# Kernel tuning notes

Hardware: AMD Instinct MI355X
Metric: run time of the kernel (lower is better)

## Reference

```python
import jax, jax.numpy as jnp
import numpy as np

LAMBDA = 10.0      # sinkhorn_lambda from init_kwargs
N_ITERS = 100      # fixed Sinkhorn iteration count
B, T_MAX, D_MAX = 256, 256, 256
TP, DP = T_MAX + 1, D_MAX + 1   # expanded with births/deaths row+col
L = TP * DP                      # padded flat output length per example
EPS = 1e-12


def setup_inputs() -> dict:
    key = jax.random.key(0)
    k1, k2, k3 = jax.random.split(key, 3)
    affinity_scores = jax.random.uniform(k1, (B, T_MAX, D_MAX), dtype=jnp.float32)
    num_detections = jax.random.randint(k2, (B,), 32, D_MAX + 1, dtype=jnp.int32)
    num_tracklets = jax.random.randint(k3, (B,), 32, T_MAX + 1, dtype=jnp.int32)
    return {
        "affinity_scores": affinity_scores,
        "num_detections": num_detections,
        "num_tracklets": num_tracklets,
    }


def _sinkhorn_transport(aff, nd, nt):
    """Masked Sinkhorn on the expanded (nt+1)x(nd+1) matrix, padded to [TP,DP]."""
    r = jnp.arange(TP)
    c = jnp.arange(DP)
    row_valid = r <= nt          # nt tracklet rows + 1 births/deaths row
    col_valid = c <= nd
    interior = (r[:, None] < nt) & (c[None, :] < nd)
    aff_pad = jnp.pad(aff, ((0, 1), (0, 1)))
    aff_e = jnp.where(interior, aff_pad, 0.0)   # dummy row/col have affinity 0
    mask = (row_valid[:, None] & col_valid[None, :]).astype(aff.dtype)
    # cost = -affinity  =>  kernel K = exp(-lambda * cost) = exp(lambda * affinity)
    K = jnp.exp(LAMBDA * aff_e) * mask
    ndf = nd.astype(aff.dtype)
    ntf = nt.astype(aff.dtype)
    # target marginals: [1,...,1, length] on valid entries, 0 on padding
    row_sums = jnp.where(r < nt, 1.0, jnp.where(r == nt, ndf, 0.0))
    col_sums = jnp.where(c < nd, 1.0, jnp.where(c == nd, ntf, 0.0))
    u0 = jnp.zeros((TP,), aff.dtype)
    v0 = col_valid.astype(aff.dtype)

    def body(carry, _):
        u, v = carry
        u = jnp.where(row_valid, row_sums / (K @ v + EPS), 0.0)
        v = jnp.where(col_valid, col_sums / (K.T @ u + EPS), 0.0)
        return (u, v), None

    (u, v), _ = jax.lax.scan(body, (u0, v0), None, length=N_ITERS)
    transport = u[:, None] * K * v[None, :]
    return transport, interior, row_valid, col_valid


def _single(aff, nd, nt):
    transport, interior, row_valid, col_valid = _sinkhorn_transport(aff, nd, nt)
    r = jnp.arange(TP)
    c = jnp.arange(DP)

    # hard assignment on transport[:-1,:-1] (valid interior): mutual argmax
    neg_inf = jnp.array(-jnp.inf, transport.dtype)
    t_in = jnp.where(interior, transport, neg_inf)
    row_max = jnp.max(t_in, axis=1, keepdims=True)
    col_max = jnp.max(t_in, axis=0, keepdims=True)
    assign_in = interior & (t_in == row_max) & (t_in == col_max)
    # births/deaths: unmatched tracklets -> death col nd; unmatched detections -> birth row nt
    row_has = jnp.any(assign_in, axis=1)
    col_has = jnp.any(assign_in, axis=0)
    deaths = (r[:, None] < nt) & (c[None, :] == nd) & (~row_has)[:, None]
    births = (r[:, None] == nt) & (c[None, :] < nd) & (~col_has)[None, :]
    assignment = assign_in | deaths | births

    # flatten the (nt+1)x(nd+1) valid submatrix row-major, zero-pad to length L
    k = jnp.arange(L)
    length = (nt + 1) * (nd + 1)
    rr = jnp.clip(k // (nd + 1), 0, T_MAX)
    cc = k % (nd + 1)
    valid = k < length
    t_flat = jnp.where(valid, transport[rr, cc], 0.0)
    a_flat = jnp.where(valid, assignment[rr, cc], False)
    return t_flat, a_flat


def reference(affinity_scores, num_detections, num_tracklets):
    t_flat, a_flat = jax.vmap(_single)(affinity_scores, num_detections, num_tracklets)
    return t_flat, a_flat
```

## Files before the change

### kernel.cpp

```cpp
#include <hip/hip_runtime.h>


#define T_MAX   256
#define L_FLAT  (257 * 257)
#define N_ITERS 100
#define LAMBDA_F 10.0f
#define EPS_F    1e-12f

#define QX1  0xB1
#define QX2  0x4E
#define ROR4 0x124
#define ROR8 0x128

template<int CTRL>
__device__ __forceinline__ float dpp_addf(float x) {
    int t = __builtin_amdgcn_update_dpp(0, __float_as_int(x), CTRL, 0xF, 0xF, true);
    return x + __int_as_float(t);
}
template<int CTRL>
__device__ __forceinline__ float dpp_maxf(float x) {
    int t = __builtin_amdgcn_update_dpp(0, __float_as_int(x), CTRL, 0xF, 0xF, true);
    return fmaxf(x, __int_as_float(t));
}
template<int CTRL>
__device__ __forceinline__ int dpp_ori(int x) {
    int t = __builtin_amdgcn_update_dpp(0, x, CTRL, 0xF, 0xF, true);
    return x | t;
}
__device__ __forceinline__ float swz16_addf(float x) {
    return x + __int_as_float(__builtin_amdgcn_ds_swizzle(__float_as_int(x), 0x401F));
}
__device__ __forceinline__ float swz16_maxf(float x) {
    return fmaxf(x, __int_as_float(__builtin_amdgcn_ds_swizzle(__float_as_int(x), 0x401F)));
}
__device__ __forceinline__ int swz16_ori(int x) {
    return x | __builtin_amdgcn_ds_swizzle(x, 0x401F);
}
__device__ __forceinline__ float sel4(float a, float b, float c, float d, int rg) {
    float lo = (rg & 1) ? b : a;
    float hi = (rg & 1) ? d : c;
    return (rg & 2) ? hi : lo;
}

__global__ __launch_bounds__(1024) void assoc_sinkhorn_kernel(
    const float* __restrict__ aff,
    const int*   __restrict__ ndet,
    const int*   __restrict__ ntrk,
    float*       __restrict__ out_t,
    float*       __restrict__ out_a)
{
    const int b   = blockIdx.x;
    const int nd  = ndet[b];
    const int nt  = ntrk[b];
    const int tid = threadIdx.x;
    const int w   = tid >> 6;
    const int l   = tid & 63;
    const int rg  = l & 3;
    const int cg  = l >> 2;
    const int R0  = (w << 4) + (rg << 2);
    const int C0  = cg << 4;

    __shared__ __align__(16) float red[16 * 256];
    __shared__ __align__(16) float varr[256];
    __shared__ __align__(16) float cmax_s[256];
    __shared__ __align__(16) float supart[16];
    __shared__ __align__(16) float svpart[2][4];
    __shared__ float sc_vbd;
    __shared__ float sc_ubd;

    float K[4][16];
    {
        const float* Ab = aff + (size_t)b * (T_MAX * T_MAX);
        #pragma unroll
        for (int i = 0; i < 4; ++i) {
            const int r = R0 + i;
            const float* row = Ab + (size_t)r * T_MAX + C0;
            #pragma unroll
            for (int k = 0; k < 4; ++k) {
                const float4 x = *reinterpret_cast<const float4*>(row + 4 * k);
                const float a4[4] = {x.x, x.y, x.z, x.w};
                #pragma unroll
                for (int e = 0; e < 4; ++e) {
                    const int j = 4 * k + e;
                    const bool interior = (r < nt) && ((C0 + j) < nd);
                    K[i][j] = interior ? expf(LAMBDA_F * a4[e]) : 0.0f;
                }
            }
        }
    }

    if (tid < 256) varr[tid] = (tid < nd) ? 1.0f : 0.0f;
    if (tid == 0) {
        sc_vbd = 1.0f;
        svpart[0][0] = (float)nd; svpart[0][1] = 0.f; svpart[0][2] = 0.f; svpart[0][3] = 0.f;
    }
    __syncthreads();

    float u[4] = {0.f, 0.f, 0.f, 0.f};
    float vbd_reg = 1.0f;

    for (int it = 0; it < N_ITERS; ++it) {
        const float vbd = sc_vbd;
        float v[16];
        {
            const float4 a0 = *reinterpret_cast<const float4*>(&varr[C0]);
            const float4 a1 = *reinterpret_cast<const float4*>(&varr[C0 + 4]);
            const float4 a2 = *reinterpret_cast<const float4*>(&varr[C0 + 8]);
            const float4 a3 = *reinterpret_cast<const float4*>(&varr[C0 + 12]);
            v[0]=a0.x; v[1]=a0.y; v[2]=a0.z; v[3]=a0.w;
            v[4]=a1.x; v[5]=a1.y; v[6]=a1.z; v[7]=a1.w;
            v[8]=a2.x; v[9]=a2.y; v[10]=a2.z; v[11]=a2.w;
            v[12]=a3.x; v[13]=a3.y; v[14]=a3.z; v[15]=a3.w;
        }
        float p[4];
        #pragma unroll
        for (int i = 0; i < 4; ++i) {
            float s = 0.f;
            #pragma unroll
            for (int j = 0; j < 16; ++j) s = fmaf(K[i][j], v[j], s);
            p[i] = s;
        }
        #pragma unroll
        for (int i = 0; i < 4; ++i) p[i] = dpp_addf<ROR4>(p[i]);
        #pragma unroll
        for (int i = 0; i < 4; ++i) p[i] = dpp_addf<ROR8>(p[i]);
        #pragma unroll
        for (int i = 0; i < 4; ++i) p[i] = swz16_addf(p[i]);
        #pragma unroll
        for (int i = 0; i < 4; ++i) p[i] += __shfl_xor(p[i], 32, 64);
        #pragma unroll
        for (int i = 0; i < 4; ++i)
            u[i] = ((R0 + i) < nt) ? 1.0f / (p[i] + vbd + EPS_F) : 0.0f;

        {
            float su = (u[0] + u[1]) + (u[2] + u[3]);
            su = dpp_addf<QX1>(su);
            su = dpp_addf<QX2>(su);
            if (l == 0) supart[w] = su;
        }

        float q[16];
        #pragma unroll
        for (int j = 0; j < 16; ++j) {
            float s = fmaf(K[0][j], u[0], 0.f);
            s = fmaf(K[1][j], u[1], s);
            s = fmaf(K[2][j], u[2], s);
            q[j] = fmaf(K[3][j], u[3], s);
        }
        #pragma unroll
        for (int j = 0; j < 16; ++j) q[j] = dpp_addf<QX1>(q[j]);
        #pragma unroll
        for (int j = 0; j < 16; ++j) q[j] = dpp_addf<QX2>(q[j]);
        {
            float4 o;
            o.x = sel4(q[0], q[4], q[8],  q[12], rg);
            o.y = sel4(q[1], q[5], q[9],  q[13], rg);
            o.z = sel4(q[2], q[6], q[10], q[14], rg);
            o.w = sel4(q[3], q[7], q[11], q[15], rg);
            *reinterpret_cast<float4*>(&red[w * 256 + C0 + (rg << 2)]) = o;
        }
        __syncthreads();

        if (tid < 256) {
            const int p_rd = it & 1;
            const float4 sv4 = *reinterpret_cast<const float4*>(&svpart[p_rd][0]);
            const float Sv = (sv4.x + sv4.y) + (sv4.z + sv4.w);
            const float ubd = (float)nd / (Sv + vbd_reg + EPS_F);

            float s0 = 0.f, s1 = 0.f, s2 = 0.f, s3 = 0.f;
            #pragma unroll
            for (int k = 0; k < 16; k += 4) {
                s0 += red[k * 256 + tid];
                s1 += red[(k + 1) * 256 + tid];
                s2 += red[(k + 2) * 256 + tid];
                s3 += red[(k + 3) * 256 + tid];
            }
            const float s = (s0 + s1) + (s2 + s3);

            const float4 p0 = *reinterpret_cast<const float4*>(&supart[0]);
            const float4 p1 = *reinterpret_cast<const float4*>(&supart[4]);
            const float4 p2 = *reinterpret_cast<const float4*>(&supart[8]);
            const float4 p3 = *reinterpret_cast<const float4*>(&supart[12]);
            const float Su = ((p0.x+p0.y)+(p0.z+p0.w)) + ((p1.x+p1.y)+(p1.z+p1.w))
                           + ((p2.x+p2.y)+(p2.z+p2.w)) + ((p3.x+p3.y)+(p3.z+p3.w));

            const float vn = (tid < nd) ? 1.0f / (s + ubd + EPS_F) : 0.0f;
            varr[tid] = vn;

            const float vbd_new = (float)nt / (Su + ubd + EPS_F);
            vbd_reg = vbd_new;
            if (tid == 0) { sc_vbd = vbd_new; sc_ubd = ubd; }

            float sv = vn;
            sv = dpp_addf<QX1>(sv);
            sv = dpp_addf<QX2>(sv);
            sv = dpp_addf<ROR4>(sv);
            sv = dpp_addf<ROR8>(sv);
            sv = swz16_addf(sv);
            sv += __shfl_xor(sv, 32, 64);
            if (l == 0) svpart[p_rd ^ 1][w] = sv;
        }
        __syncthreads();
    }

    const float vbdF = sc_vbd;
    const float ubdF = sc_ubd;
    float v[16];
    {
        const float4 a0 = *reinterpret_cast<const float4*>(&varr[C0]);
        const float4 a1 = *reinterpret_cast<const float4*>(&varr[C0 + 4]);
        const float4 a2 = *reinterpret_cast<const float4*>(&varr[C0 + 8]);
        const float4 a3 = *reinterpret_cast<const float4*>(&varr[C0 + 12]);
        v[0]=a0.x; v[1]=a0.y; v[2]=a0.z; v[3]=a0.w;
        v[4]=a1.x; v[5]=a1.y; v[6]=a1.z; v[7]=a1.w;
        v[8]=a2.x; v[9]=a2.y; v[10]=a2.z; v[11]=a2.w;
        v[12]=a3.x; v[13]=a3.y; v[14]=a3.z; v[15]=a3.w;
    }
    #pragma unroll
    for (int i = 0; i < 4; ++i) {
        #pragma unroll
        for (int j = 0; j < 16; ++j) K[i][j] = u[i] * K[i][j] * v[j];
    }

    float m[4];
    #pragma unroll
    for (int i = 0; i < 4; ++i) {
        float mm = K[i][0];
        #pragma unroll
        for (int j = 1; j < 16; ++j) mm = fmaxf(mm, K[i][j]);
        m[i] = mm;
    }
    #pragma unroll
    for (int i = 0; i < 4; ++i) m[i] = dpp_maxf<ROR4>(m[i]);
    #pragma unroll
    for (int i = 0; i < 4; ++i) m[i] = dpp_maxf<ROR8>(m[i]);
    #pragma unroll
    for (int i = 0; i < 4; ++i) m[i] = swz16_maxf(m[i]);
    #pragma unroll
    for (int i = 0; i < 4; ++i) m[i] = fmaxf(m[i], __shfl_xor(m[i], 32, 64));

    {
        float cmx[16];
        #pragma unroll
        for (int j = 0; j < 16; ++j)
            cmx[j] = fmaxf(fmaxf(K[0][j], K[1][j]), fmaxf(K[2][j], K[3][j]));
        #pragma unroll
        for (int j = 0; j < 16; ++j) cmx[j] = dpp_maxf<QX1>(cmx[j]);
        #pragma unroll
        for (int j = 0; j < 16; ++j) cmx[j] = dpp_maxf<QX2>(cmx[j]);
        float4 o;
        o.x = sel4(cmx[0], cmx[4], cmx[8],  cmx[12], rg);
        o.y = sel4(cmx[1], cmx[5], cmx[9],  cmx[13], rg);
        o.z = sel4(cmx[2], cmx[6], cmx[10], cmx[14], rg);
        o.w = sel4(cmx[3], cmx[7], cmx[11], cmx[15], rg);
        *reinterpret_cast<float4*>(&red[w * 256 + C0 + (rg << 2)]) = o;
    }
    __syncthreads();
    if (tid < 256) {
        float mm = red[tid];
        #pragma unroll
        for (int k = 1; k < 16; ++k) mm = fmaxf(mm, red[k * 256 + tid]);
        cmax_s[tid] = mm;
    }
    __syncthreads();

    float cm[16];
    {
        const float4 a0 = *reinterpret_cast<const float4*>(&cmax_s[C0]);
        const float4 a1 = *reinterpret_cast<const float4*>(&cmax_s[C0 + 4]);
        const float4 a2 = *reinterpret_cast<const float4*>(&cmax_s[C0 + 8]);
        const float4 a3 = *reinterpret_cast<const float4*>(&cmax_s[C0 + 12]);
        cm[0]=a0.x; cm[1]=a0.y; cm[2]=a0.z; cm[3]=a0.w;
        cm[4]=a1.x; cm[5]=a1.y; cm[6]=a1.z; cm[7]=a1.w;
        cm[8]=a2.x; cm[9]=a2.y; cm[10]=a2.z; cm[11]=a2.w;
        cm[12]=a3.x; cm[13]=a3.y; cm[14]=a3.z; cm[15]=a3.w;
    }
    unsigned bits[4];
    #pragma unroll
    for (int i = 0; i < 4; ++i) {
        unsigned bi = 0;
        const int r = R0 + i;
        #pragma unroll
        for (int j = 0; j < 16; ++j) {
            const int c = C0 + j;
            if ((r < nt) && (c < nd) && (K[i][j] == m[i]) && (K[i][j] == cm[j]))
                bi |= (1u << j);
        }
        bits[i] = bi;
    }
    int rh[4];
    #pragma unroll
    for (int i = 0; i < 4; ++i) rh[i] = bits[i] ? 1 : 0;
    #pragma unroll
    for (int i = 0; i < 4; ++i) rh[i] = dpp_ori<ROR4>(rh[i]);
    #pragma unroll
    for (int i = 0; i < 4; ++i) rh[i] = dpp_ori<ROR8>(rh[i]);
    #pragma unroll
    for (int i = 0; i < 4; ++i) rh[i] = swz16_ori(rh[i]);
    #pragma unroll
    for (int i = 0; i < 4; ++i) rh[i] |= __shfl_xor(rh[i], 32, 64);

    {
        const unsigned anyb = bits[0] | bits[1] | bits[2] | bits[3];
        float ch[16];
        #pragma unroll
        for (int j = 0; j < 16; ++j) ch[j] = ((anyb >> j) & 1u) ? 1.0f : 0.0f;
        #pragma unroll
        for (int j = 0; j < 16; ++j) ch[j] = dpp_maxf<QX1>(ch[j]);
        #pragma unroll
        for (int j = 0; j < 16; ++j) ch[j] = dpp_maxf<QX2>(ch[j]);
        float4 o;
        o.x = sel4(ch[0], ch[4], ch[8],  ch[12], rg);
        o.y = sel4(ch[1], ch[5], ch[9],  ch[13], rg);
        o.z = sel4(ch[2], ch[6], ch[10], ch[14], rg);
        o.w = sel4(ch[3], ch[7], ch[11], ch[15], rg);
        *reinterpret_cast<float4*>(&red[w * 256 + C0 + (rg << 2)]) = o;
    }
    __syncthreads();

    float* Ot = out_t + (size_t)b * L_FLAT;
    float* Oa = out_a + (size_t)b * L_FLAT;
    const int stride = nd + 1;

    if (tid < 256) {
        float c = red[tid];
        #pragma unroll
        for (int k = 1; k < 16; ++k) c = fmaxf(c, red[k * 256 + tid]);
        if (tid < nd) {
            const int kk = nt * stride + tid;
            Ot[kk] = ubdF * varr[tid];
            Oa[kk] = (c > 0.0f) ? 0.0f : 1.0f;
        }
    }
    if (tid == 0) {
        const int kk = nt * stride + nd;
        Ot[kk] = ubdF * vbdF;
        Oa[kk] = 0.0f;
    }
    if (cg == 0) {
        #pragma unroll
        for (int i = 0; i < 4; ++i) {
            const int r = R0 + i;
            if (r < nt) {
                const int kk = r * stride + nd;
                Ot[kk] = u[i] * vbdF;
                Oa[kk] = rh[i] ? 0.0f : 1.0f;
            }
        }
    }
    #pragma unroll
    for (int i = 0; i < 4; ++i) {
        const int r = R0 + i;
        if (r < nt) {
            const int base = r * stride;
            #pragma unroll
            for (int j = 0; j < 16; ++j) {
                const int c = C0 + j;
                if (c < nd) {
                    Ot[base + c] = K[i][j];
                    Oa[base + c] = ((bits[i] >> j) & 1u) ? 1.0f : 0.0f;
                }
            }
        }
    }
    const int length = (nt + 1) * stride;
    for (int k = length + tid; k < L_FLAT; k += 1024) {
        Ot[k] = 0.0f;
        Oa[k] = 0.0f;
    }
}

extern "C" void kernel_launch(void* const* d_in, const int* in_sizes, int n_in,
                              void* d_out, int out_size, void* d_ws, size_t ws_size,
                              hipStream_t stream)
{
    const float* aff  = (const float*)d_in[0];
    const int*   ndet = (const int*)d_in[1];
    const int*   ntrk = (const int*)d_in[2];
    const int    Bn   = in_sizes[1];
    float* out_t = (float*)d_out;
    float* out_a = out_t + (size_t)Bn * L_FLAT;
    assoc_sinkhorn_kernel<<<dim3(Bn), dim3(1024), 0, stream>>>(aff, ndet, ntrk, out_t, out_a);
}
```

Before: 444.6 us.

## Use packed FMA, fast reciprocal, and all-thread column reduction in Sinkhorn loop

```diff
diff --git a/kernel.cpp b/kernel.cpp
--- a/kernel.cpp
+++ b/kernel.cpp
@@ -1,11 +1,14 @@
 #include <hip/hip_runtime.h>
 
+
+typedef float v2f __attribute__((ext_vector_type(2)));
 
 #define T_MAX   256
 #define L_FLAT  (257 * 257)
 #define N_ITERS 100
 #define LAMBDA_F 10.0f
 #define EPS_F    1e-12f
+#define RS      260
 
 #define QX1  0xB1
 #define QX2  0x4E
@@ -36,10 +39,12 @@
 __device__ __forceinline__ int swz16_ori(int x) {
     return x | __builtin_amdgcn_ds_swizzle(x, 0x401F);
 }
-__device__ __forceinline__ float sel4(float a, float b, float c, float d, int rg) {
-    float lo = (rg & 1) ? b : a;
-    float hi = (rg & 1) ? d : c;
-    return (rg & 2) ? hi : lo;
+__device__ __forceinline__ float fast_rcp(float x) {
+#if __has_builtin(__builtin_amdgcn_rcpf)
+    return __builtin_amdgcn_rcpf(x);
+#else
+    return 1.0f / x;
+#endif
 }
 
 __global__ __launch_bounds__(1024) void assoc_sinkhorn_kernel(
@@ -60,15 +65,16 @@
     const int R0  = (w << 4) + (rg << 2);
     const int C0  = cg << 4;
 
-    __shared__ __align__(16) float red[16 * 256];
+    __shared__ __align__(16) float red[16 * RS];
     __shared__ __align__(16) float varr[256];
     __shared__ __align__(16) float cmax_s[256];
     __shared__ __align__(16) float supart[16];
-    __shared__ __align__(16) float svpart[2][4];
-    __shared__ float sc_vbd;
-    __shared__ float sc_ubd;
-
-    float K[4][16];
+    __shared__ __align__(16) float svpart[2][16];
+
+    const float ndf = (float)nd;
+    const float ntf = (float)nt;
+
+    v2f K2[4][8];
     {
         const float* Ab = aff + (size_t)b * (T_MAX * T_MAX);
         #pragma unroll
@@ -78,47 +84,48 @@
             #pragma unroll
             for (int k = 0; k < 4; ++k) {
                 const float4 x = *reinterpret_cast<const float4*>(row + 4 * k);
-                const float a4[4] = {x.x, x.y, x.z, x.w};
-                #pragma unroll
-                for (int e = 0; e < 4; ++e) {
-                    const int j = 4 * k + e;
-                    const bool interior = (r < nt) && ((C0 + j) < nd);
-                    K[i][j] = interior ? expf(LAMBDA_F * a4[e]) : 0.0f;
-                }
+                const bool rv = (r < nt);
+                const float e0 = (rv && (C0 + 4*k + 0) < nd) ? expf(LAMBDA_F * x.x) : 0.0f;
+                const float e1 = (rv && (C0 + 4*k + 1) < nd) ? expf(LAMBDA_F * x.y) : 0.0f;
+                const float e2 = (rv && (C0 + 4*k + 2) < nd) ? expf(LAMBDA_F * x.z) : 0.0f;
+                const float e3 = (rv && (C0 + 4*k + 3) < nd) ? expf(LAMBDA_F * x.w) : 0.0f;
+                K2[i][2*k + 0] = (v2f){e0, e1};
+                K2[i][2*k + 1] = (v2f){e2, e3};
             }
         }
     }
 
     if (tid < 256) varr[tid] = (tid < nd) ? 1.0f : 0.0f;
-    if (tid == 0) {
-        sc_vbd = 1.0f;
-        svpart[0][0] = (float)nd; svpart[0][1] = 0.f; svpart[0][2] = 0.f; svpart[0][3] = 0.f;
-    }
+    if (tid < 16)  svpart[0][tid] = (tid == 0) ? ndf : 0.0f;
     __syncthreads();
 
     float u[4] = {0.f, 0.f, 0.f, 0.f};
-    float vbd_reg = 1.0f;
+    float vbd = 1.0f;
+    float ubd = 0.0f;
+
+    const int s2c   = (w << 4) + (l >> 2);
+    const int s2sub = l & 3;
 
     for (int it = 0; it < N_ITERS; ++it) {
-        const float vbd = sc_vbd;
-        float v[16];
+        v2f v2[8];
         {
             const float4 a0 = *reinterpret_cast<const float4*>(&varr[C0]);
             const float4 a1 = *reinterpret_cast<const float4*>(&varr[C0 + 4]);
             const float4 a2 = *reinterpret_cast<const float4*>(&varr[C0 + 8]);
             const float4 a3 = *reinterpret_cast<const float4*>(&varr[C0 + 12]);
-            v[0]=a0.x; v[1]=a0.y; v[2]=a0.z; v[3]=a0.w;
-            v[4]=a1.x; v[5]=a1.y; v[6]=a1.z; v[7]=a1.w;
-            v[8]=a2.x; v[9]=a2.y; v[10]=a2.z; v[11]=a2.w;
-            v[12]=a3.x; v[13]=a3.y; v[14]=a3.z; v[15]=a3.w;
+            v2[0] = (v2f){a0.x, a0.y}; v2[1] = (v2f){a0.z, a0.w};
+            v2[2] = (v2f){a1.x, a1.y}; v2[3] = (v2f){a1.z, a1.w};
+            v2[4] = (v2f){a2.x, a2.y}; v2[5] = (v2f){a2.z, a2.w};
+            v2[6] = (v2f){a3.x, a3.y}; v2[7] = (v2f){a3.z, a3.w};
         }
         float p[4];
         #pragma unroll
         for (int i = 0; i < 4; ++i) {
-            float s = 0.f;
+            v2f s2 = K2[i][0] * v2[0];
             #pragma unroll
-            for (int j = 0; j < 16; ++j) s = fmaf(K[i][j], v[j], s);
-            p[i] = s;
+            for (int jj = 1; jj < 8; ++jj)
+                s2 = __builtin_elementwise_fma(K2[i][jj], v2[jj], s2);
+            p[i] = s2.x + s2.y;
         }
         #pragma unroll
         for (int i = 0; i < 4; ++i) p[i] = dpp_addf<ROR4>(p[i]);
@@ -128,9 +135,10 @@
         for (int i = 0; i < 4; ++i) p[i] = swz16_addf(p[i]);
         #pragma unroll
         for (int i = 0; i < 4; ++i) p[i] += __shfl_xor(p[i], 32, 64);
+        const float vbdE = vbd + EPS_F;
         #pragma unroll
         for (int i = 0; i < 4; ++i)
-            u[i] = ((R0 + i) < nt) ? 1.0f / (p[i] + vbd + EPS_F) : 0.0f;
+            u[i] = ((R0 + i) < nt) ? fast_rcp(p[i] + vbdE) : 0.0f;
 
         {
             float su = (u[0] + u[1]) + (u[2] + u[3]);
@@ -139,96 +147,99 @@
             if (l == 0) supart[w] = su;
         }
 
+        v2f q2[8];
+        {
+            const v2f u0 = (v2f){u[0], u[0]};
+            #pragma unroll
+            for (int jj = 0; jj < 8; ++jj) q2[jj] = K2[0][jj] * u0;
+            #pragma unroll
+            for (int i = 1; i < 4; ++i) {
+                const v2f ui = (v2f){u[i], u[i]};
+                #pragma unroll
+                for (int jj = 0; jj < 8; ++jj)
+                    q2[jj] = __builtin_elementwise_fma(K2[i][jj], ui, q2[jj]);
+            }
+        }
         float q[16];
         #pragma unroll
-        for (int j = 0; j < 16; ++j) {
-            float s = fmaf(K[0][j], u[0], 0.f);
-            s = fmaf(K[1][j], u[1], s);
-            s = fmaf(K[2][j], u[2], s);
-            q[j] = fmaf(K[3][j], u[3], s);
-        }
+        for (int jj = 0; jj < 8; ++jj) { q[2*jj] = q2[jj].x; q[2*jj + 1] = q2[jj].y; }
         #pragma unroll
         for (int j = 0; j < 16; ++j) q[j] = dpp_addf<QX1>(q[j]);
         #pragma unroll
         for (int j = 0; j < 16; ++j) q[j] = dpp_addf<QX2>(q[j]);
+        if (rg == 0) {
+            float* dst = &red[w * RS + C0];
+            *reinterpret_cast<float4*>(dst)      = make_float4(q[0],  q[1],  q[2],  q[3]);
+            *reinterpret_cast<float4*>(dst + 4)  = make_float4(q[4],  q[5],  q[6],  q[7]);
+            *reinterpret_cast<float4*>(dst + 8)  = make_float4(q[8],  q[9],  q[10], q[11]);
+            *reinterpret_cast<float4*>(dst + 12) = make_float4(q[12], q[13], q[14], q[15]);
+        }
+        __syncthreads();
+
         {
-            float4 o;
-            o.x = sel4(q[0], q[4], q[8],  q[12], rg);
-            o.y = sel4(q[1], q[5], q[9],  q[13], rg);
-            o.z = sel4(q[2], q[6], q[10], q[14], rg);
-            o.w = sel4(q[3], q[7], q[11], q[15], rg);
-            *reinterpret_cast<float4*>(&red[w * 256 + C0 + (rg << 2)]) = o;
+            const int p_rd = it & 1;
+            float s0 = red[(4*s2sub + 0) * RS + s2c];
+            float s1 = red[(4*s2sub + 1) * RS + s2c];
+            float s2 = red[(4*s2sub + 2) * RS + s2c];
+            float s3 = red[(4*s2sub + 3) * RS + s2c];
+            float s = (s0 + s1) + (s2 + s3);
+            s = dpp_addf<QX1>(s);
+            s = dpp_addf<QX2>(s);
+
+            const float4 a0 = *reinterpret_cast<const float4*>(&supart[0]);
+            const float4 a1 = *reinterpret_cast<const float4*>(&supart[4]);
+            const float4 a2 = *reinterpret_cast<const float4*>(&supart[8]);
+            const float4 a3 = *reinterpret_cast<const float4*>(&supart[12]);
+            const float Su = (((a0.x+a0.y)+(a0.z+a0.w)) + ((a1.x+a1.y)+(a1.z+a1.w)))
+                           + (((a2.x+a2.y)+(a2.z+a2.w)) + ((a3.x+a3.y)+(a3.z+a3.w)));
+            const float4 b0 = *reinterpret_cast<const float4*>(&svpart[p_rd][0]);
+            const float4 b1 = *reinterpret_cast<const float4*>(&svpart[p_rd][4]);
+            const float4 b2 = *reinterpret_cast<const float4*>(&svpart[p_rd][8]);
+            const float4 b3 = *reinterpret_cast<const float4*>(&svpart[p_rd][12]);
+            const float Sv = (((b0.x+b0.y)+(b0.z+b0.w)) + ((b1.x+b1.y)+(b1.z+b1.w)))
+                           + (((b2.x+b2.y)+(b2.z+b2.w)) + ((b3.x+b3.y)+(b3.z+b3.w)));
+
+            const float ubd_new = ndf * fast_rcp(Sv + vbd + EPS_F);
+            const float vn = (s2c < nd) ? fast_rcp(s + ubd_new + EPS_F) : 0.0f;
+            if (s2sub == 0) varr[s2c] = vn;
+            vbd = ntf * fast_rcp(Su + ubd_new + EPS_F);
+            ubd = ubd_new;
+
+            float x = (s2sub == 0) ? vn : 0.0f;
+            x = dpp_addf<ROR4>(x);
+            x = dpp_addf<ROR8>(x);
+            x = swz16_addf(x);
+            x += __shfl_xor(x, 32, 64);
+            if (l == 0) svpart[p_rd ^ 1][w] = x;
         }
         __syncthreads();
-
-        if (tid < 256) {
-            const int p_rd = it & 1;
-            const float4 sv4 = *reinterpret_cast<const float4*>(&svpart[p_rd][0]);
-            const float Sv = (sv4.x + sv4.y) + (sv4.z + sv4.w);
-            const float ubd = (float)nd / (Sv + vbd_reg + EPS_F);
-
-            float s0 = 0.f, s1 = 0.f, s2 = 0.f, s3 = 0.f;
-            #pragma unroll
-            for (int k = 0; k < 16; k += 4) {
-                s0 += red[k * 256 + tid];
-                s1 += red[(k + 1) * 256 + tid];
-                s2 += red[(k + 2) * 256 + tid];
-                s3 += red[(k + 3) * 256 + tid];
-            }
-            const float s = (s0 + s1) + (s2 + s3);
-
-            const float4 p0 = *reinterpret_cast<const float4*>(&supart[0]);
-            const float4 p1 = *reinterpret_cast<const float4*>(&supart[4]);
-            const float4 p2 = *reinterpret_cast<const float4*>(&supart[8]);
-            const float4 p3 = *reinterpret_cast<const float4*>(&supart[12]);
-            const float Su = ((p0.x+p0.y)+(p0.z+p0.w)) + ((p1.x+p1.y)+(p1.z+p1.w))
-                           + ((p2.x+p2.y)+(p2.z+p2.w)) + ((p3.x+p3.y)+(p3.z+p3.w));
-
-            const float vn = (tid < nd) ? 1.0f / (s + ubd + EPS_F) : 0.0f;
-            varr[tid] = vn;
-
-            const float vbd_new = (float)nt / (Su + ubd + EPS_F);
-            vbd_reg = vbd_new;
-            if (tid == 0) { sc_vbd = vbd_new; sc_ubd = ubd; }
-
-            float sv = vn;
-            sv = dpp_addf<QX1>(sv);
-            sv = dpp_addf<QX2>(sv);
-            sv = dpp_addf<ROR4>(sv);
-            sv = dpp_addf<ROR8>(sv);
-            sv = swz16_addf(sv);
-            sv += __shfl_xor(sv, 32, 64);
-            if (l == 0) svpart[p_rd ^ 1][w] = sv;
-        }
-        __syncthreads();
-    }
-
-    const float vbdF = sc_vbd;
-    const float ubdF = sc_ubd;
-    float v[16];
+    }
+
+    v2f v2[8];
     {
         const float4 a0 = *reinterpret_cast<const float4*>(&varr[C0]);
         const float4 a1 = *reinterpret_cast<const float4*>(&varr[C0 + 4]);
         const float4 a2 = *reinterpret_cast<const float4*>(&varr[C0 + 8]);
         const float4 a3 = *reinterpret_cast<const float4*>(&varr[C0 + 12]);
-        v[0]=a0.x; v[1]=a0.y; v[2]=a0.z; v[3]=a0.w;
-        v[4]=a1.x; v[5]=a1.y; v[6]=a1.z; v[7]=a1.w;
-        v[8]=a2.x; v[9]=a2.y; v[10]=a2.z; v[11]=a2.w;
-        v[12]=a3.x; v[13]=a3.y; v[14]=a3.z; v[15]=a3.w;
+        v2[0] = (v2f){a0.x, a0.y}; v2[1] = (v2f){a0.z, a0.w};
+        v2[2] = (v2f){a1.x, a1.y}; v2[3] = (v2f){a1.z, a1.w};
+        v2[4] = (v2f){a2.x, a2.y}; v2[5] = (v2f){a2.z, a2.w};
+        v2[6] = (v2f){a3.x, a3.y}; v2[7] = (v2f){a3.z, a3.w};
     }
     #pragma unroll
     for (int i = 0; i < 4; ++i) {
-        #pragma unroll
-        for (int j = 0; j < 16; ++j) K[i][j] = u[i] * K[i][j] * v[j];
+        const v2f ui = (v2f){u[i], u[i]};
+        #pragma unroll
+        for (int jj = 0; jj < 8; ++jj) K2[i][jj] = ui * K2[i][jj] * v2[jj];
     }
 
     float m[4];
     #pragma unroll
     for (int i = 0; i < 4; ++i) {
-        float mm = K[i][0];
-        #pragma unroll
-        for (int j = 1; j < 16; ++j) mm = fmaxf(mm, K[i][j]);
-        m[i] = mm;
+        v2f mm2 = __builtin_elementwise_max(K2[i][0], K2[i][1]);
+        #pragma unroll
+        for (int jj = 2; jj < 8; ++jj) mm2 = __builtin_elementwise_max(mm2, K2[i][jj]);
+        m[i] = fmaxf(mm2.x, mm2.y);
     }
     #pragma unroll
     for (int i = 0; i < 4; ++i) m[i] = dpp_maxf<ROR4>(m[i]);
@@ -242,24 +253,29 @@
     {
         float cmx[16];
         #pragma unroll
-        for (int j = 0; j < 16; ++j)
-            cmx[j] = fmaxf(fmaxf(K[0][j], K[1][j]), fmaxf(K[2][j], K[3][j]));
+        for (int jj = 0; jj < 8; ++jj) {
+            v2f c2 = __builtin_elementwise_max(
+                         __builtin_elementwise_max(K2[0][jj], K2[1][jj]),
+                         __builtin_elementwise_max(K2[2][jj], K2[3][jj]));
+            cmx[2*jj] = c2.x; cmx[2*jj + 1] = c2.y;
+        }
         #pragma unroll
         for (int j = 0; j < 16; ++j) cmx[j] = dpp_maxf<QX1>(cmx[j]);
         #pragma unroll
         for (int j = 0; j < 16; ++j) cmx[j] = dpp_maxf<QX2>(cmx[j]);
-        float4 o;
-        o.x = sel4(cmx[0], cmx[4], cmx[8],  cmx[12], rg);
-        o.y = sel4(cmx[1], cmx[5], cmx[9],  cmx[13], rg);
-        o.z = sel4(cmx[2], cmx[6], cmx[10], cmx[14], rg);
-        o.w = sel4(cmx[3], cmx[7], cmx[11], cmx[15], rg);
-        *reinterpret_cast<float4*>(&red[w * 256 + C0 + (rg << 2)]) = o;
+        if (rg == 0) {
+            float* dst = &red[w * RS + C0];
+            *reinterpret_cast<float4*>(dst)      = make_float4(cmx[0],  cmx[1],  cmx[2],  cmx[3]);
+            *reinterpret_cast<float4*>(dst + 4)  = make_float4(cmx[4],  cmx[5],  cmx[6],  cmx[7]);
+            *reinterpret_cast<float4*>(dst + 8)  = make_float4(cmx[8],  cmx[9],  cmx[10], cmx[11]);
+            *reinterpret_cast<float4*>(dst + 12) = make_float4(cmx[12], cmx[13], cmx[14], cmx[15]);
+        }
     }
     __syncthreads();
     if (tid < 256) {
         float mm = red[tid];
         #pragma unroll
-        for (int k = 1; k < 16; ++k) mm = fmaxf(mm, red[k * 256 + tid]);
+        for (int k = 1; k < 16; ++k) mm = fmaxf(mm, red[k * RS + tid]);
         cmax_s[tid] = mm;
     }
     __syncthreads();
@@ -281,10 +297,11 @@
         unsigned bi = 0;
         const int r = R0 + i;
         #pragma unroll
-        for (int j = 0; j < 16; ++j) {
-            const int c = C0 + j;
-            if ((r < nt) && (c < nd) && (K[i][j] == m[i]) && (K[i][j] == cm[j]))
-                bi |= (1u << j);
+        for (int jj = 0; jj < 8; ++jj) {
+            const float kx = K2[i][jj].x, ky = K2[i][jj].y;
+            const int c0j = C0 + 2*jj, c1j = C0 + 2*jj + 1;
+            if ((r < nt) && (c0j < nd) && (kx == m[i]) && (kx == cm[2*jj]))     bi |= (1u << (2*jj));
+            if ((r < nt) && (c1j < nd) && (ky == m[i]) && (ky == cm[2*jj + 1])) bi |= (1u << (2*jj + 1));
         }
         bits[i] = bi;
     }
@@ -309,12 +326,13 @@
         for (int j = 0; j < 16; ++j) ch[j] = dpp_maxf<QX1>(ch[j]);
         #pragma unroll
         for (int j = 0; j < 16; ++j) ch[j] = dpp_maxf<QX2>(ch[j]);
-        float4 o;
-        o.x = sel4(ch[0], ch[4], ch[8],  ch[12], rg);
-        o.y = sel4(ch[1], ch[5], ch[9],  ch[13], rg);
-        o.z = sel4(ch[2], ch[6], ch[10], ch[14], rg);
-        o.w = sel4(ch[3], ch[7], ch[11], ch[15], rg);
-        *reinterpret_cast<float4*>(&red[w * 256 + C0 + (rg << 2)]) = o;
+        if (rg == 0) {
+            float* dst = &red[w * RS + C0];
+            *reinterpret_cast<float4*>(dst)      = make_float4(ch[0],  ch[1],  ch[2],  ch[3]);
+            *reinterpret_cast<float4*>(dst + 4)  = make_float4(ch[4],  ch[5],  ch[6],  ch[7]);
+            *reinterpret_cast<float4*>(dst + 8)  = make_float4(ch[8],  ch[9],  ch[10], ch[11]);
+            *reinterpret_cast<float4*>(dst + 12) = make_float4(ch[12], ch[13], ch[14], ch[15]);
+        }
     }
     __syncthreads();
 
@@ -325,16 +343,16 @@
     if (tid < 256) {
         float c = red[tid];
         #pragma unroll
-        for (int k = 1; k < 16; ++k) c = fmaxf(c, red[k * 256 + tid]);
+        for (int k = 1; k < 16; ++k) c = fmaxf(c, red[k * RS + tid]);
         if (tid < nd) {
             const int kk = nt * stride + tid;
-            Ot[kk] = ubdF * varr[tid];
+            Ot[kk] = ubd * varr[tid];
             Oa[kk] = (c > 0.0f) ? 0.0f : 1.0f;
         }
     }
     if (tid == 0) {
         const int kk = nt * stride + nd;
-        Ot[kk] = ubdF * vbdF;
+        Ot[kk] = ubd * vbd;
         Oa[kk] = 0.0f;
     }
     if (cg == 0) {
@@ -343,7 +361,7 @@
             const int r = R0 + i;
             if (r < nt) {
                 const int kk = r * stride + nd;
-                Ot[kk] = u[i] * vbdF;
+                Ot[kk] = u[i] * vbd;
                 Oa[kk] = rh[i] ? 0.0f : 1.0f;
             }
         }
@@ -354,11 +372,15 @@
         if (r < nt) {
             const int base = r * stride;
             #pragma unroll
-            for (int j = 0; j < 16; ++j) {
-                const int c = C0 + j;
-                if (c < nd) {
-                    Ot[base + c] = K[i][j];
-                    Oa[base + c] = ((bits[i] >> j) & 1u) ? 1.0f : 0.0f;
+            for (int jj = 0; jj < 8; ++jj) {
+                const int c0j = C0 + 2*jj, c1j = c0j + 1;
+                if (c0j < nd) {
+                    Ot[base + c0j] = K2[i][jj].x;
+                    Oa[base + c0j] = ((bits[i] >> (2*jj)) & 1u) ? 1.0f : 0.0f;
+                }
+                if (c1j < nd) {
+                    Ot[base + c1j] = K2[i][jj].y;
+                    Oa[base + c1j] = ((bits[i] >> (2*jj + 1)) & 1u) ? 1.0f : 0.0f;
                 }
             }
         }
```

After: 503.7 us. 1.13x slower.
